# Optimization experiments

Measured on AMD Instinct MI355X. Metric: run time of the kernel, lower is better.

The kernel has to match this reference:

```python
import jax, jax.numpy as jnp
import numpy as np

T, K, E, D, F = 16, 8, 64, 2048, 1024  # tokens, top_k, experts, hidden, intermediate


def setup_inputs() -> dict:
    key = jax.random.key(0)
    k1, k2, k3, k4, k5 = jax.random.split(key, 5)
    hidden_states = jax.random.normal(k1, (T, D), dtype=jnp.float32)
    top_k_index = jax.random.randint(k2, (T, K), 0, E, dtype=jnp.int64)
    # routing weights (already summed/normalized per the module's contract)
    top_k_weights = jax.random.uniform(k3, (T, K), dtype=jnp.float32) / K
    # dense dequantized per-expert weights (up: D->F, down: F->D, no bias)
    W_up = jax.random.normal(k4, (E, D, F), dtype=jnp.float32) * 0.02
    W_down = jax.random.normal(k5, (E, F, D), dtype=jnp.float32) * 0.02
    return {
        "hidden_states": hidden_states,
        "top_k_index": top_k_index,
        "top_k_weights": top_k_weights,
        "W_up": W_up,
        "W_down": W_down,
    }


def reference(hidden_states, top_k_index, top_k_weights, W_up, W_down):
    num_experts = W_up.shape[0]
    # route[t, e] = sum_k top_k_weights[t, k] * (top_k_index[t, k] == e)
    route = jnp.sum(
        jax.nn.one_hot(top_k_index, num_experts, dtype=top_k_weights.dtype)
        * top_k_weights[..., None],
        axis=1,
    )  # [T, E]
    # up_proj for every expert on every token (few tokens -> cheap, weight-bound)
    h = jnp.einsum("td,edf->etf", hidden_states, W_up)  # [E, T, F]
    a = jnp.square(jax.nn.relu(h))  # relu^2 activation (NemotronH non-gated MoE)
    # down_proj then weighted combine; experts not routed get zero weight
    out = jnp.einsum("etf,efd,te->td", a, W_down, route)  # [T, D]
    return out.astype(hidden_states.dtype)
```

## Files before the change

kernel.cpp:

```cpp
#include <hip/hip_runtime.h>

#define T_TOK 16
#define K_TOP 8
#define NEXP  64
#define DHID  2048
#define FINT  1024

typedef unsigned int   uint_t;
typedef unsigned short ushort_t;
typedef float f32x4 __attribute__((ext_vector_type(4)));

#define ROUTE_OFF 0u
#define AIDX_OFF  4096u
#define NA_OFF    (AIDX_OFF + 256u)
#define XT_OFF    8192u
#define HPART_OFF 262144u
#define HPART_STRIDE ((size_t)NEXP * FINT * T_TOK)
#define ABUF_OFF  (HPART_OFF + 8388608u)
#define OPART_OFF (ABUF_OFF + 2097152u)

__device__ __forceinline__ ushort_t f2bf(float f) {
    uint_t u = __builtin_bit_cast(uint_t, f);
    u += 0x7FFFu + ((u >> 16) & 1u);
    return (ushort_t)(u >> 16);
}
__device__ __forceinline__ uint_t pk2(float lo, float hi) {
    return (uint_t)f2bf(lo) | ((uint_t)f2bf(hi) << 16);
}
__device__ __forceinline__ float bf_lo(uint_t v) { return __builtin_bit_cast(float, v << 16); }
__device__ __forceinline__ float bf_hi(uint_t v) { return __builtin_bit_cast(float, v & 0xFFFF0000u); }

__global__ void k_prep(const float* __restrict__ x, const int* __restrict__ idx,
                       const float* __restrict__ w, float* __restrict__ xT,
                       float* __restrict__ route, int* __restrict__ aidx,
                       int* __restrict__ nA) {
    const int tid = threadIdx.x;
    const int d = blockIdx.x * 64 + (tid & 63);
    const int tq = tid >> 6;
    float4 v;
    v.x = x[(tq * 4 + 0) * DHID + d];
    v.y = x[(tq * 4 + 1) * DHID + d];
    v.z = x[(tq * 4 + 2) * DHID + d];
    v.w = x[(tq * 4 + 3) * DHID + d];
    *reinterpret_cast<float4*>(xT + d * T_TOK + tq * 4) = v;

    if (blockIdx.x != 0) return;
    __shared__ float r[NEXP * T_TOK];
    __shared__ int is64_s;
    if (tid == 0) {
        int allz = 1;
        for (int i = 1; i < 128; i += 2) allz &= (idx[i] == 0);
        is64_s = allz;
    }
    __syncthreads();
    const int is64 = is64_s;
    for (int i = tid; i < NEXP * T_TOK; i += 256) {
        const int e = i >> 4, t = i & 15;
        float s = 0.f;
#pragma unroll
        for (int k = 0; k < K_TOP; ++k) {
            const int flat = t * K_TOP + k;
            const int ev = is64 ? idx[2 * flat] : idx[flat];
            if (ev == e) s += w[flat];
        }
        r[i] = s;
        route[i] = s;
    }
    __syncthreads();
    if (tid == 0) {
        int n = 0;
        for (int e = 0; e < NEXP; ++e) {
            float s = 0.f;
            for (int t = 0; t < T_TOK; ++t) s += r[e * T_TOK + t];
            if (s != 0.f) aidx[n++] = e;
        }
        *nA = n;
    }
}

#define FMA4(t, xs)                              \
    acc0[t] = fmaf((xs), w4.x, acc0[t]);         \
    acc1[t] = fmaf((xs), w4.y, acc1[t]);         \
    acc2[t] = fmaf((xs), w4.z, acc2[t]);         \
    acc3[t] = fmaf((xs), w4.w, acc3[t]);
#define FMA_PAIR(u, t0_)                                        \
    { const float xl = bf_lo(u), xh = bf_hi(u);                 \
      FMA4(t0_, xl) FMA4((t0_) + 1, xh) }
#define STEP(jj, B)                                                         \
    { const uint4 q0 = xqw[(jj) * 2]; const uint4 q1 = xqw[(jj) * 2 + 1];   \
      const f32x4 w4 = (B);                                                 \
      FMA_PAIR(q0.x, 0) FMA_PAIR(q0.y, 2) FMA_PAIR(q0.z, 4) FMA_PAIR(q0.w, 6) \
      FMA_PAIR(q1.x, 8) FMA_PAIR(q1.y, 10) FMA_PAIR(q1.z, 12) FMA_PAIR(q1.w, 14) }
#define LDW(j) __builtin_nontemporal_load(wrow + (size_t)(j) * WSTEP)

#define RW(reg)                                                         \
    { uint_t* p = lds_u + (reg) * 2048 + lane;                          \
      _Pragma("unroll") for (int tp = 0; tp < 8; ++tp) {                \
          p[(0 * 8 + tp) * 64] = pk2(acc0[2 * tp], acc0[2 * tp + 1]);   \
          p[(1 * 8 + tp) * 64] = pk2(acc1[2 * tp], acc1[2 * tp + 1]);   \
          p[(2 * 8 + tp) * 64] = pk2(acc2[2 * tp], acc2[2 * tp + 1]);   \
          p[(3 * 8 + tp) * 64] = pk2(acc3[2 * tp], acc3[2 * tp + 1]); } }
#define RR(reg)                                                         \
    { const uint_t* p = lds_u + (reg) * 2048 + lane;                    \
      _Pragma("unroll") for (int tp = 0; tp < 8; ++tp) {                \
          uint_t u;                                                     \
          u = p[(0 * 8 + tp) * 64]; acc0[2 * tp] += bf_lo(u); acc0[2 * tp + 1] += bf_hi(u); \
          u = p[(1 * 8 + tp) * 64]; acc1[2 * tp] += bf_lo(u); acc1[2 * tp + 1] += bf_hi(u); \
          u = p[(2 * 8 + tp) * 64]; acc2[2 * tp] += bf_lo(u); acc2[2 * tp + 1] += bf_hi(u); \
          u = p[(3 * 8 + tp) * 64]; acc3[2 * tp] += bf_lo(u); acc3[2 * tp + 1] += bf_hi(u); } }

__global__ __launch_bounds__(1024, 4) void k_up(
    const float* __restrict__ xT, const float* __restrict__ Wu,
    const int* __restrict__ aidx, const int* __restrict__ nAp,
    ushort_t* __restrict__ h_part) {
    const int b = blockIdx.x;
    if (b >= 4 * (*nAp)) return;
    const int e = aidx[b >> 2];
    const int dr = b & 3;
    const int tid = threadIdx.x;
    const int wid = tid >> 6, lane = tid & 63;
    const int dsub = wid >> 2, fq = wid & 3;

    __shared__ __align__(16) uint_t lds_u[16384];

    {
        const float4* src = reinterpret_cast<const float4*>(xT + (size_t)dr * 512 * T_TOK);
        uint2* dst = reinterpret_cast<uint2*>(lds_u);
#pragma unroll
        for (int i = 0; i < 2; ++i) {
            const float4 v = src[tid * 2 + i];
            dst[tid * 2 + i] = make_uint2(pk2(v.x, v.y), pk2(v.z, v.w));
        }
    }
    __syncthreads();

    float acc0[16] = {}, acc1[16] = {}, acc2[16] = {}, acc3[16] = {};

    const f32x4* wrow = reinterpret_cast<const f32x4*>(
        Wu + (size_t)e * ((size_t)DHID * FINT)
           + (size_t)(dr * 512 + dsub * 128) * FINT + fq * 256 + lane * 4);
    const size_t WSTEP = FINT / 4;
    const uint4* xqw = reinterpret_cast<const uint4*>(lds_u) + (size_t)dsub * 256;

    f32x4 b0 = LDW(0), b1 = LDW(1), b2 = LDW(2), b3 = LDW(3);
    for (int j = 0; j < 128; j += 4) {
        const bool pf = (j < 124);
        STEP(j + 0, b0) if (pf) b0 = LDW(j + 4);
        STEP(j + 1, b1) if (pf) b1 = LDW(j + 5);
        STEP(j + 2, b2) if (pf) b2 = LDW(j + 6);
        STEP(j + 3, b3) if (pf) b3 = LDW(j + 7);
    }

    __syncthreads();
    if (dsub >= 2) RW(fq * 2 + dsub - 2)
    __syncthreads();
    if (dsub < 2) RR(fq * 2 + dsub)
    __syncthreads();
    if (dsub == 1) RW(fq)
    __syncthreads();
    if (dsub == 0) {
        RR(fq)
        uint4* hp = reinterpret_cast<uint4*>(
            h_part + ((size_t)(dr * NEXP + e) * FINT + fq * 256 + lane * 4) * T_TOK);
        uint4 o;
#define ST_COL(A, k0)                                                        \
        o.x = pk2(A[0], A[1]);   o.y = pk2(A[2], A[3]);                      \
        o.z = pk2(A[4], A[5]);   o.w = pk2(A[6], A[7]);                      \
        hp[k0] = o;                                                          \
        o.x = pk2(A[8], A[9]);   o.y = pk2(A[10], A[11]);                    \
        o.z = pk2(A[12], A[13]); o.w = pk2(A[14], A[15]);                    \
        hp[k0 + 1] = o;
        ST_COL(acc0, 0) ST_COL(acc1, 2) ST_COL(acc2, 4) ST_COL(acc3, 6)
#undef ST_COL
    }
}

__global__ void k_act(const ushort_t* __restrict__ h_part, const float* __restrict__ route,
                      ushort_t* __restrict__ a_buf) {
    const int e = blockIdx.y;
    const int i = blockIdx.x * 256 + threadIdx.x;
    const size_t base = (size_t)e * (FINT * T_TOK) + (size_t)i * 8;

    float s[8] = {};
#pragma unroll
    for (int dr = 0; dr < 4; ++dr) {
        const uint4 hv = *reinterpret_cast<const uint4*>(h_part + dr * HPART_STRIDE + base);
        s[0] += bf_lo(hv.x); s[1] += bf_hi(hv.x);
        s[2] += bf_lo(hv.y); s[3] += bf_hi(hv.y);
        s[4] += bf_lo(hv.z); s[5] += bf_hi(hv.z);
        s[6] += bf_lo(hv.w); s[7] += bf_hi(hv.w);
    }
    const int t0 = (i & 1) * 8;
    const float* r = route + e * T_TOK + t0;
    uint4 o;
    float h0, h1;
    h0 = fmaxf(s[0], 0.f); h1 = fmaxf(s[1], 0.f);
    o.x = pk2(r[0] * h0 * h0, r[1] * h1 * h1);
    h0 = fmaxf(s[2], 0.f); h1 = fmaxf(s[3], 0.f);
    o.y = pk2(r[2] * h0 * h0, r[3] * h1 * h1);
    h0 = fmaxf(s[4], 0.f); h1 = fmaxf(s[5], 0.f);
    o.z = pk2(r[4] * h0 * h0, r[5] * h1 * h1);
    h0 = fmaxf(s[6], 0.f); h1 = fmaxf(s[7], 0.f);
    o.w = pk2(r[6] * h0 * h0, r[7] * h1 * h1);
    *reinterpret_cast<uint4*>(a_buf + base) = o;
}

__global__ __launch_bounds__(1024, 4) void k_down(
    const ushort_t* __restrict__ a_buf, const float* __restrict__ Wd,
    const int* __restrict__ aidx, const int* __restrict__ nAp,
    ushort_t* __restrict__ out_part) {
    const int b = blockIdx.x;
    if (b >= 4 * (*nAp)) return;
    const int e = aidx[b >> 2];
    const int fr = b & 3;
    const int tid = threadIdx.x;
    const int wid = tid >> 6, lane = tid & 63;
    const int fs = wid >> 3, dq = wid & 7;

    __shared__ __align__(16) uint_t lds_u[16384];

    {
        const uint4* src = reinterpret_cast<const uint4*>(
            a_buf + ((size_t)e * FINT + fr * 256) * T_TOK);
        reinterpret_cast<uint4*>(lds_u)[tid] = src[tid];
    }
    __syncthreads();

    float acc0[16] = {}, acc1[16] = {}, acc2[16] = {}, acc3[16] = {};

    const int d0 = dq * 256 + lane * 4;
    const f32x4* wrow = reinterpret_cast<const f32x4*>(
        Wd + (size_t)e * ((size_t)FINT * DHID)
           + (size_t)(fr * 256 + fs * 128) * DHID + d0);
    const size_t WSTEP = DHID / 4;
    const uint4* xqw = reinterpret_cast<const uint4*>(lds_u) + (size_t)fs * 256;

    f32x4 b0 = LDW(0), b1 = LDW(1), b2 = LDW(2), b3 = LDW(3);
    for (int j = 0; j < 128; j += 4) {
        const bool pf = (j < 124);
        STEP(j + 0, b0) if (pf) b0 = LDW(j + 4);
        STEP(j + 1, b1) if (pf) b1 = LDW(j + 5);
        STEP(j + 2, b2) if (pf) b2 = LDW(j + 6);
        STEP(j + 3, b3) if (pf) b3 = LDW(j + 7);
    }

    __syncthreads();
    if (fs == 1) RW(dq)
    __syncthreads();
    if (fs == 0) {
        RR(dq)
        ushort_t* op = out_part + ((size_t)(e * 4 + fr) * T_TOK) * DHID + d0;
#pragma unroll
        for (int t = 0; t < 16; ++t) {
            uint2 u;
            u.x = pk2(acc0[t], acc1[t]);
            u.y = pk2(acc2[t], acc3[t]);
            *reinterpret_cast<uint2*>(op + (size_t)t * DHID) = u;
        }
    }
}

__global__ void k_comb(const ushort_t* __restrict__ out_part, const int* __restrict__ aidx,
                       const int* __restrict__ nAp, float* __restrict__ out) {
    const int i = blockIdx.x * 256 + threadIdx.x;
    const int nA = *nAp;
    const int t = i >> 9;
    const int d = (i & 511) * 4;
    const size_t off = (size_t)t * DHID + d;
    float s0 = 0.f, s1 = 0.f, s2 = 0.f, s3 = 0.f;
    for (int a = 0; a < nA; ++a) {
        const int e = aidx[a];
#pragma unroll
        for (int fr = 0; fr < 4; ++fr) {
            const uint2 v = *reinterpret_cast<const uint2*>(
                out_part + (size_t)(e * 4 + fr) * (T_TOK * DHID) + off);
            s0 += bf_lo(v.x); s1 += bf_hi(v.x);
            s2 += bf_lo(v.y); s3 += bf_hi(v.y);
        }
    }
    *reinterpret_cast<float4*>(out + off) = make_float4(s0, s1, s2, s3);
}

extern "C" void kernel_launch(void* const* d_in, const int* in_sizes, int n_in,
                              void* d_out, int out_size, void* d_ws, size_t ws_size,
                              hipStream_t stream) {
    (void)in_sizes; (void)n_in; (void)out_size; (void)ws_size;
    const float* x   = (const float*)d_in[0];
    const int*   idx = (const int*)d_in[1];
    const float* w   = (const float*)d_in[2];
    const float* Wu  = (const float*)d_in[3];
    const float* Wd  = (const float*)d_in[4];
    float* out = (float*)d_out;

    char* ws = (char*)d_ws;
    float*    route    = (float*)(ws + ROUTE_OFF);
    int*      aidx     = (int*)(ws + AIDX_OFF);
    int*      nA       = (int*)(ws + NA_OFF);
    float*    xT       = (float*)(ws + XT_OFF);
    ushort_t* h_part   = (ushort_t*)(ws + HPART_OFF);
    ushort_t* a_buf    = (ushort_t*)(ws + ABUF_OFF);
    ushort_t* out_part = (ushort_t*)(ws + OPART_OFF);

    k_prep<<<DHID / 64, 256, 0, stream>>>(x, idx, w, xT, route, aidx, nA);
    k_up<<<4 * NEXP, 1024, 0, stream>>>(xT, Wu, aidx, nA, h_part);
    k_act<<<dim3(8, NEXP), 256, 0, stream>>>(h_part, route, a_buf);
    k_down<<<4 * NEXP, 1024, 0, stream>>>(a_buf, Wd, aidx, nA, out_part);
    k_comb<<<(T_TOK * DHID / 4) / 256, 256, 0, stream>>>(out_part, aidx, nA, out);
}
```

Before: 205.5 us.

## Fuse up-projection, activation and down-projection into one kernel per expert quarter

Merges k_up, k_act and k_down into a single k_main kernel. Each block computes a full-D reduction for one 256-wide F slice of one expert, using a 16-wave LDS tree reduction, then applies relu^2 and the routing weight in LDS. It then streams the matching W_down rows, so h_part and a_buf no longer go through global memory and two launches are dropped. In exchange each block now reads the whole of x and does a deeper LDS reduction with more barriers. The per-block balance between up and down weight streaming also changes, and x is now converted to bf16 in k_prep.

```diff
diff --git a/kernel.cpp b/kernel.cpp
--- a/kernel.cpp
+++ b/kernel.cpp
@@ -12,12 +12,9 @@
 
 #define ROUTE_OFF 0u
 #define AIDX_OFF  4096u
-#define NA_OFF    (AIDX_OFF + 256u)
-#define XT_OFF    8192u
-#define HPART_OFF 262144u
-#define HPART_STRIDE ((size_t)NEXP * FINT * T_TOK)
-#define ABUF_OFF  (HPART_OFF + 8388608u)
-#define OPART_OFF (ABUF_OFF + 2097152u)
+#define NA_OFF    4352u
+#define XTBF_OFF  8192u
+#define OPART_OFF 131072u
 
 __device__ __forceinline__ ushort_t f2bf(float f) {
     uint_t u = __builtin_bit_cast(uint_t, f);
@@ -31,7 +28,7 @@
 __device__ __forceinline__ float bf_hi(uint_t v) { return __builtin_bit_cast(float, v & 0xFFFF0000u); }
 
 __global__ void k_prep(const float* __restrict__ x, const int* __restrict__ idx,
-                       const float* __restrict__ w, float* __restrict__ xT,
+                       const float* __restrict__ w, uint_t* __restrict__ xt_bf,
                        float* __restrict__ route, int* __restrict__ aidx,
                        int* __restrict__ nA) {
     const int tid = threadIdx.x;
@@ -42,7 +39,8 @@
     v.y = x[(tq * 4 + 1) * DHID + d];
     v.z = x[(tq * 4 + 2) * DHID + d];
     v.w = x[(tq * 4 + 3) * DHID + d];
-    *reinterpret_cast<float4*>(xT + d * T_TOK + tq * 4) = v;
+    *reinterpret_cast<uint2*>(xt_bf + d * 8 + tq * 2) =
+        make_uint2(pk2(v.x, v.y), pk2(v.z, v.w));
 
     if (blockIdx.x != 0) return;
     __shared__ float r[NEXP * T_TOK];
@@ -92,6 +90,14 @@
       FMA_PAIR(q0.x, 0) FMA_PAIR(q0.y, 2) FMA_PAIR(q0.z, 4) FMA_PAIR(q0.w, 6) \
       FMA_PAIR(q1.x, 8) FMA_PAIR(q1.y, 10) FMA_PAIR(q1.z, 12) FMA_PAIR(q1.w, 14) }
 #define LDW(j) __builtin_nontemporal_load(wrow + (size_t)(j) * WSTEP)
+#define STREAM128()                                                \
+    { f32x4 b0 = LDW(0), b1 = LDW(1), b2 = LDW(2), b3 = LDW(3);    \
+      for (int j = 0; j < 128; j += 4) {                           \
+          const bool pf = (j < 124);                               \
+          STEP(j + 0, b0) if (pf) b0 = LDW(j + 4);                 \
+          STEP(j + 1, b1) if (pf) b1 = LDW(j + 5);                 \
+          STEP(j + 2, b2) if (pf) b2 = LDW(j + 6);                 \
+          STEP(j + 3, b3) if (pf) b3 = LDW(j + 7); } }
 
 #define RW(reg)                                                         \
     { uint_t* p = lds_u + (reg) * 2048 + lane;                          \
@@ -109,147 +115,97 @@
           u = p[(2 * 8 + tp) * 64]; acc2[2 * tp] += bf_lo(u); acc2[2 * tp + 1] += bf_hi(u); \
           u = p[(3 * 8 + tp) * 64]; acc3[2 * tp] += bf_lo(u); acc3[2 * tp + 1] += bf_hi(u); } }
 
-__global__ __launch_bounds__(1024, 4) void k_up(
-    const float* __restrict__ xT, const float* __restrict__ Wu,
-    const int* __restrict__ aidx, const int* __restrict__ nAp,
-    ushort_t* __restrict__ h_part) {
-    const int b = blockIdx.x;
-    if (b >= 4 * (*nAp)) return;
-    const int e = aidx[b >> 2];
-    const int dr = b & 3;
-    const int tid = threadIdx.x;
-    const int wid = tid >> 6, lane = tid & 63;
-    const int dsub = wid >> 2, fq = wid & 3;
-
-    __shared__ __align__(16) uint_t lds_u[16384];
-
-    {
-        const float4* src = reinterpret_cast<const float4*>(xT + (size_t)dr * 512 * T_TOK);
-        uint2* dst = reinterpret_cast<uint2*>(lds_u);
-#pragma unroll
-        for (int i = 0; i < 2; ++i) {
-            const float4 v = src[tid * 2 + i];
-            dst[tid * 2 + i] = make_uint2(pk2(v.x, v.y), pk2(v.z, v.w));
-        }
-    }
-    __syncthreads();
-
-    float acc0[16] = {}, acc1[16] = {}, acc2[16] = {}, acc3[16] = {};
-
-    const f32x4* wrow = reinterpret_cast<const f32x4*>(
-        Wu + (size_t)e * ((size_t)DHID * FINT)
-           + (size_t)(dr * 512 + dsub * 128) * FINT + fq * 256 + lane * 4);
-    const size_t WSTEP = FINT / 4;
-    const uint4* xqw = reinterpret_cast<const uint4*>(lds_u) + (size_t)dsub * 256;
-
-    f32x4 b0 = LDW(0), b1 = LDW(1), b2 = LDW(2), b3 = LDW(3);
-    for (int j = 0; j < 128; j += 4) {
-        const bool pf = (j < 124);
-        STEP(j + 0, b0) if (pf) b0 = LDW(j + 4);
-        STEP(j + 1, b1) if (pf) b1 = LDW(j + 5);
-        STEP(j + 2, b2) if (pf) b2 = LDW(j + 6);
-        STEP(j + 3, b3) if (pf) b3 = LDW(j + 7);
-    }
-
-    __syncthreads();
-    if (dsub >= 2) RW(fq * 2 + dsub - 2)
-    __syncthreads();
-    if (dsub < 2) RR(fq * 2 + dsub)
-    __syncthreads();
-    if (dsub == 1) RW(fq)
-    __syncthreads();
-    if (dsub == 0) {
-        RR(fq)
-        uint4* hp = reinterpret_cast<uint4*>(
-            h_part + ((size_t)(dr * NEXP + e) * FINT + fq * 256 + lane * 4) * T_TOK);
-        uint4 o;
-#define ST_COL(A, k0)                                                        \
-        o.x = pk2(A[0], A[1]);   o.y = pk2(A[2], A[3]);                      \
-        o.z = pk2(A[4], A[5]);   o.w = pk2(A[6], A[7]);                      \
-        hp[k0] = o;                                                          \
-        o.x = pk2(A[8], A[9]);   o.y = pk2(A[10], A[11]);                    \
-        o.z = pk2(A[12], A[13]); o.w = pk2(A[14], A[15]);                    \
-        hp[k0 + 1] = o;
-        ST_COL(acc0, 0) ST_COL(acc1, 2) ST_COL(acc2, 4) ST_COL(acc3, 6)
-#undef ST_COL
-    }
-}
-
-__global__ void k_act(const ushort_t* __restrict__ h_part, const float* __restrict__ route,
-                      ushort_t* __restrict__ a_buf) {
-    const int e = blockIdx.y;
-    const int i = blockIdx.x * 256 + threadIdx.x;
-    const size_t base = (size_t)e * (FINT * T_TOK) + (size_t)i * 8;
-
-    float s[8] = {};
-#pragma unroll
-    for (int dr = 0; dr < 4; ++dr) {
-        const uint4 hv = *reinterpret_cast<const uint4*>(h_part + dr * HPART_STRIDE + base);
-        s[0] += bf_lo(hv.x); s[1] += bf_hi(hv.x);
-        s[2] += bf_lo(hv.y); s[3] += bf_hi(hv.y);
-        s[4] += bf_lo(hv.z); s[5] += bf_hi(hv.z);
-        s[6] += bf_lo(hv.w); s[7] += bf_hi(hv.w);
-    }
-    const int t0 = (i & 1) * 8;
-    const float* r = route + e * T_TOK + t0;
-    uint4 o;
-    float h0, h1;
-    h0 = fmaxf(s[0], 0.f); h1 = fmaxf(s[1], 0.f);
-    o.x = pk2(r[0] * h0 * h0, r[1] * h1 * h1);
-    h0 = fmaxf(s[2], 0.f); h1 = fmaxf(s[3], 0.f);
-    o.y = pk2(r[2] * h0 * h0, r[3] * h1 * h1);
-    h0 = fmaxf(s[4], 0.f); h1 = fmaxf(s[5], 0.f);
-    o.z = pk2(r[4] * h0 * h0, r[5] * h1 * h1);
-    h0 = fmaxf(s[6], 0.f); h1 = fmaxf(s[7], 0.f);
-    o.w = pk2(r[6] * h0 * h0, r[7] * h1 * h1);
-    *reinterpret_cast<uint4*>(a_buf + base) = o;
-}
-
-__global__ __launch_bounds__(1024, 4) void k_down(
-    const ushort_t* __restrict__ a_buf, const float* __restrict__ Wd,
+#define TREE16()                                   \
+    __syncthreads();                               \
+    if (wid >= 8) RW(wid - 8)                      \
+    __syncthreads();                               \
+    if (wid < 8) RR(wid)                           \
+    __syncthreads();                               \
+    if (wid >= 4 && wid < 8) RW(wid - 4)           \
+    __syncthreads();                               \
+    if (wid < 4) RR(wid)                           \
+    __syncthreads();                               \
+    if (wid >= 2 && wid < 4) RW(wid - 2)           \
+    __syncthreads();                               \
+    if (wid < 2) RR(wid)                           \
+    __syncthreads();                               \
+    if (wid == 1) RW(0)                            \
+    __syncthreads();
+
+__global__ __launch_bounds__(1024, 4) void k_main(
+    const uint_t* __restrict__ xt_bf, const float* __restrict__ Wu,
+    const float* __restrict__ Wd, const float* __restrict__ route,
     const int* __restrict__ aidx, const int* __restrict__ nAp,
     ushort_t* __restrict__ out_part) {
     const int b = blockIdx.x;
     if (b >= 4 * (*nAp)) return;
     const int e = aidx[b >> 2];
-    const int fr = b & 3;
+    const int q = b & 3;
     const int tid = threadIdx.x;
     const int wid = tid >> 6, lane = tid & 63;
+
+    __shared__ __align__(16) uint_t lds_u[16384];
+    __shared__ __align__(16) uint_t a_lds[2048];
+
+    {
+        const uint4* src = reinterpret_cast<const uint4*>(xt_bf);
+        uint4* dst = reinterpret_cast<uint4*>(lds_u);
+        dst[tid] = src[tid];
+        dst[tid + 1024] = src[tid + 1024];
+        dst[tid + 2048] = src[tid + 2048];
+        dst[tid + 3072] = src[tid + 3072];
+    }
+    __syncthreads();
+
+    float acc0[16] = {}, acc1[16] = {}, acc2[16] = {}, acc3[16] = {};
+
+    {
+        const f32x4* wrow = reinterpret_cast<const f32x4*>(
+            Wu + (size_t)e * ((size_t)DHID * FINT)
+               + (size_t)(wid * 128) * FINT + q * 256 + lane * 4);
+        const size_t WSTEP = FINT / 4;
+        const uint4* xqw = reinterpret_cast<const uint4*>(lds_u) + (size_t)wid * 256;
+        STREAM128()
+    }
+    TREE16()
+    if (wid == 0) {
+        RR(0)
+        float rt[16];
+#pragma unroll
+        for (int t = 0; t < 16; ++t) rt[t] = route[e * T_TOK + t];
+#define ACT(A, t) (rt[t] * fmaxf(A[t], 0.f) * fmaxf(A[t], 0.f))
+        uint4* ap = reinterpret_cast<uint4*>(a_lds) + (size_t)lane * 8;
+        uint4 o;
+#define ST_COL(A, j2)                                                            \
+        o.x = pk2(ACT(A, 0), ACT(A, 1));   o.y = pk2(ACT(A, 2), ACT(A, 3));      \
+        o.z = pk2(ACT(A, 4), ACT(A, 5));   o.w = pk2(ACT(A, 6), ACT(A, 7));      \
+        ap[j2] = o;                                                              \
+        o.x = pk2(ACT(A, 8), ACT(A, 9));   o.y = pk2(ACT(A, 10), ACT(A, 11));    \
+        o.z = pk2(ACT(A, 12), ACT(A, 13)); o.w = pk2(ACT(A, 14), ACT(A, 15));    \
+        ap[j2 + 1] = o;
+        ST_COL(acc0, 0) ST_COL(acc1, 2) ST_COL(acc2, 4) ST_COL(acc3, 6)
+#undef ST_COL
+#undef ACT
+    }
+    __syncthreads();
+
+#pragma unroll
+    for (int t = 0; t < 16; ++t) { acc0[t] = 0.f; acc1[t] = 0.f; acc2[t] = 0.f; acc3[t] = 0.f; }
     const int fs = wid >> 3, dq = wid & 7;
-
-    __shared__ __align__(16) uint_t lds_u[16384];
-
     {
-        const uint4* src = reinterpret_cast<const uint4*>(
-            a_buf + ((size_t)e * FINT + fr * 256) * T_TOK);
-        reinterpret_cast<uint4*>(lds_u)[tid] = src[tid];
-    }
-    __syncthreads();
-
-    float acc0[16] = {}, acc1[16] = {}, acc2[16] = {}, acc3[16] = {};
-
-    const int d0 = dq * 256 + lane * 4;
-    const f32x4* wrow = reinterpret_cast<const f32x4*>(
-        Wd + (size_t)e * ((size_t)FINT * DHID)
-           + (size_t)(fr * 256 + fs * 128) * DHID + d0);
-    const size_t WSTEP = DHID / 4;
-    const uint4* xqw = reinterpret_cast<const uint4*>(lds_u) + (size_t)fs * 256;
-
-    f32x4 b0 = LDW(0), b1 = LDW(1), b2 = LDW(2), b3 = LDW(3);
-    for (int j = 0; j < 128; j += 4) {
-        const bool pf = (j < 124);
-        STEP(j + 0, b0) if (pf) b0 = LDW(j + 4);
-        STEP(j + 1, b1) if (pf) b1 = LDW(j + 5);
-        STEP(j + 2, b2) if (pf) b2 = LDW(j + 6);
-        STEP(j + 3, b3) if (pf) b3 = LDW(j + 7);
-    }
-
+        const f32x4* wrow = reinterpret_cast<const f32x4*>(
+            Wd + (size_t)e * ((size_t)FINT * DHID)
+               + (size_t)(q * 256 + fs * 128) * DHID + dq * 256 + lane * 4);
+        const size_t WSTEP = DHID / 4;
+        const uint4* xqw = reinterpret_cast<const uint4*>(a_lds) + (size_t)fs * 256;
+        STREAM128()
+    }
     __syncthreads();
     if (fs == 1) RW(dq)
     __syncthreads();
     if (fs == 0) {
         RR(dq)
-        ushort_t* op = out_part + ((size_t)(e * 4 + fr) * T_TOK) * DHID + d0;
+        ushort_t* op = out_part + (size_t)b * (T_TOK * DHID) + dq * 256 + lane * 4;
 #pragma unroll
         for (int t = 0; t < 16; ++t) {
             uint2 u;
@@ -260,23 +216,19 @@
     }
 }
 
-__global__ void k_comb(const ushort_t* __restrict__ out_part, const int* __restrict__ aidx,
-                       const int* __restrict__ nAp, float* __restrict__ out) {
+__global__ void k_comb(const ushort_t* __restrict__ out_part, const int* __restrict__ nAp,
+                       float* __restrict__ out) {
     const int i = blockIdx.x * 256 + threadIdx.x;
-    const int nA = *nAp;
+    const int nS = 4 * (*nAp);
     const int t = i >> 9;
     const int d = (i & 511) * 4;
     const size_t off = (size_t)t * DHID + d;
     float s0 = 0.f, s1 = 0.f, s2 = 0.f, s3 = 0.f;
-    for (int a = 0; a < nA; ++a) {
-        const int e = aidx[a];
-#pragma unroll
-        for (int fr = 0; fr < 4; ++fr) {
-            const uint2 v = *reinterpret_cast<const uint2*>(
-                out_part + (size_t)(e * 4 + fr) * (T_TOK * DHID) + off);
-            s0 += bf_lo(v.x); s1 += bf_hi(v.x);
-            s2 += bf_lo(v.y); s3 += bf_hi(v.y);
-        }
+    for (int s = 0; s < nS; ++s) {
+        const uint2 v = *reinterpret_cast<const uint2*>(
+            out_part + (size_t)s * (T_TOK * DHID) + off);
+        s0 += bf_lo(v.x); s1 += bf_hi(v.x);
+        s2 += bf_lo(v.y); s3 += bf_hi(v.y);
     }
     *reinterpret_cast<float4*>(out + off) = make_float4(s0, s1, s2, s3);
 }
@@ -296,14 +248,10 @@
     float*    route    = (float*)(ws + ROUTE_OFF);
     int*      aidx     = (int*)(ws + AIDX_OFF);
     int*      nA       = (int*)(ws + NA_OFF);
-    float*    xT       = (float*)(ws + XT_OFF);
-    ushort_t* h_part   = (ushort_t*)(ws + HPART_OFF);
-    ushort_t* a_buf    = (ushort_t*)(ws + ABUF_OFF);
+    uint_t*   xt_bf    = (uint_t*)(ws + XTBF_OFF);
     ushort_t* out_part = (ushort_t*)(ws + OPART_OFF);
 
-    k_prep<<<DHID / 64, 256, 0, stream>>>(x, idx, w, xT, route, aidx, nA);
-    k_up<<<4 * NEXP, 1024, 0, stream>>>(xT, Wu, aidx, nA, h_part);
-    k_act<<<dim3(8, NEXP), 256, 0, stream>>>(h_part, route, a_buf);
-    k_down<<<4 * NEXP, 1024, 0, stream>>>(a_buf, Wd, aidx, nA, out_part);
-    k_comb<<<(T_TOK * DHID / 4) / 256, 256, 0, stream>>>(out_part, aidx, nA, out);
-}
+    k_prep<<<DHID / 64, 256, 0, stream>>>(x, idx, w, xt_bf, route, aidx, nA);
+    k_main<<<4 * NEXP, 1024, 0, stream>>>(xt_bf, Wu, Wd, route, aidx, nA, out_part);
+    k_comb<<<(T_TOK * DHID / 4) / 256, 256, 0, stream>>>(out_part, nA, out);
+}
```

Measured after the change: 270.8 us. 31.7% more time.
